# Performance work log

Hardware: AMD Instinct MI355X
Metric: run time of the kernel (lower is better)

The kernel has to match this reference:

```python
import jax, jax.numpy as jnp
import numpy as np

N_NODES = 100000
N_EDGES = 1600000
IN_F, H_F, OUT_F = 32, 32, 16


def setup_inputs() -> dict:
    key = jax.random.key(0)
    ks = jax.random.split(key, 9)
    x = jax.random.normal(ks[0], (N_NODES, IN_F), dtype=jnp.float32)
    src = jax.random.randint(ks[1], (N_EDGES,), 0, N_NODES, dtype=jnp.int32)
    dst = jax.random.randint(ks[2], (N_EDGES,), 0, N_NODES, dtype=jnp.int32)
    W1 = jax.random.normal(ks[3], (IN_F, H_F), dtype=jnp.float32) / np.sqrt(IN_F)
    b1 = jax.random.normal(ks[4], (H_F,), dtype=jnp.float32) * 0.01
    W2 = jax.random.normal(ks[5], (H_F, H_F), dtype=jnp.float32) / np.sqrt(H_F)
    b2 = jax.random.normal(ks[6], (H_F,), dtype=jnp.float32) * 0.01
    W3 = jax.random.normal(ks[7], (H_F, OUT_F), dtype=jnp.float32) / np.sqrt(H_F)
    b3 = jax.random.normal(ks[8], (OUT_F,), dtype=jnp.float32) * 0.01
    return {"x": x, "src": src, "dst": dst,
            "W1": W1, "b1": b1, "W2": W2, "b2": b2, "W3": W3, "b3": b3}


def _gcn_layer(h, src, dst, W, b, num_nodes):
    # copy_u + sum: each dst node accumulates the sum of its source neighbors' features,
    # then dense Linear. Gather-scatter over the edge list (no dense adjacency).
    agg = jax.ops.segment_sum(h[src], dst, num_segments=num_nodes)  # [N, F_in]
    return agg @ W + b


def _leaky_relu(v, slope=0.1):
    return jnp.where(v >= 0, v, slope * v)


def reference(x, src, dst, W1, b1, W2, b2, W3, b3) -> jnp.ndarray:
    n = x.shape[0]
    h = _leaky_relu(_gcn_layer(x, src, dst, W1, b1, n))
    h = _leaky_relu(_gcn_layer(h, src, dst, W2, b2, n))
    return _gcn_layer(h, src, dst, W3, b3, n)  # [N, OUT_F]
```

## Files before the change

kernel.cpp:

```cpp
#include <hip/hip_runtime.h>


#define RANGE_BITS 7
#define RANGE      128
#define MAXBK      1024
#define CHUNK      8192
#define FILL_T     512
#define CSR_T      256
#define CSR_CAP    4096

typedef unsigned short ushort_t;

__device__ __forceinline__ ushort_t f32_to_bf16(float x) {
    unsigned u = __float_as_uint(x);
    u += 0x7fffu + ((u >> 16) & 1u);
    return (ushort_t)(u >> 16);
}
__device__ __forceinline__ float bf16_to_f32(ushort_t h) {
    return __uint_as_float(((unsigned)h) << 16);
}


__global__ void zero_kernel(int* __restrict__ p, int count) {
    int i = blockIdx.x * blockDim.x + threadIdx.x;
    if (i < count) p[i] = 0;
}

__global__ void hist_kernel(const int* __restrict__ dst, int* __restrict__ ghist,
                            int nE, int nbk) {
    __shared__ int h[MAXBK];
    const int tid = threadIdx.x;
    for (int i = tid; i < nbk; i += blockDim.x) h[i] = 0;
    __syncthreads();
    const int stride = gridDim.x * blockDim.x;
    const int nv = nE >> 2;
    const uint4* d4 = (const uint4*)dst;
    for (int i = blockIdx.x * blockDim.x + tid; i < nv; i += stride) {
        uint4 v = d4[i];
        atomicAdd(&h[v.x >> RANGE_BITS], 1);
        atomicAdd(&h[v.y >> RANGE_BITS], 1);
        atomicAdd(&h[v.z >> RANGE_BITS], 1);
        atomicAdd(&h[v.w >> RANGE_BITS], 1);
    }
    for (int e = (nv << 2) + blockIdx.x * blockDim.x + tid; e < nE; e += stride)
        atomicAdd(&h[dst[e] >> RANGE_BITS], 1);
    __syncthreads();
    for (int i = tid; i < nbk; i += blockDim.x) {
        int c = h[i];
        if (c) atomicAdd(&ghist[i], c);
    }
}

__global__ void scan_kernel(int* __restrict__ ghist, int* __restrict__ boff,
                            int* __restrict__ gcur, int nbk) {
    __shared__ int lds[MAXBK];
    const int tid = threadIdx.x;
    for (int i = tid; i < nbk; i += blockDim.x) lds[i] = ghist[i];
    __syncthreads();
    for (int o = 1; o < nbk; o <<= 1) {
        int v = (tid >= o && tid < nbk) ? lds[tid - o] : 0;
        __syncthreads();
        if (tid < nbk) lds[tid] += v;
        __syncthreads();
    }
    if (tid < nbk) {
        int ex = (tid == 0) ? 0 : lds[tid - 1];
        boff[tid] = ex;
        gcur[tid] = ex;
        if (tid == nbk - 1) boff[nbk] = lds[tid];
    }
}

__global__ __launch_bounds__(FILL_T)
void fill_kernel(const int* __restrict__ src, const int* __restrict__ dst,
                 int* __restrict__ gcur, unsigned* __restrict__ edata,
                 int nE, int nbk) {
    __shared__ int cnt[MAXBK];
    __shared__ int base[MAXBK];
    const int tid = threadIdx.x;
    const int c0 = blockIdx.x * CHUNK;
    const int c1 = min(c0 + CHUNK, nE);
    for (int i = tid; i < nbk; i += FILL_T) cnt[i] = 0;
    __syncthreads();
    {
        const int full4 = (c1 - c0) >> 2;
        const uint4* d4 = (const uint4*)(dst + c0);
        for (int i = tid; i < full4; i += FILL_T) {
            uint4 v = d4[i];
            atomicAdd(&cnt[v.x >> RANGE_BITS], 1);
            atomicAdd(&cnt[v.y >> RANGE_BITS], 1);
            atomicAdd(&cnt[v.z >> RANGE_BITS], 1);
            atomicAdd(&cnt[v.w >> RANGE_BITS], 1);
        }
        for (int e = c0 + (full4 << 2) + tid; e < c1; e += FILL_T)
            atomicAdd(&cnt[dst[e] >> RANGE_BITS], 1);
    }
    __syncthreads();
    for (int i = tid; i < nbk; i += FILL_T) {
        int c = cnt[i];
        base[i] = c ? atomicAdd(&gcur[i], c) : 0;
        cnt[i] = 0;
    }
    __syncthreads();
    {
        const int full4 = (c1 - c0) >> 2;
        const uint4* d4 = (const uint4*)(dst + c0);
        const uint4* s4 = (const uint4*)(src + c0);
        for (int i = tid; i < full4; i += FILL_T) {
            uint4 dv = d4[i];
            uint4 sv = s4[i];
#pragma unroll
            for (int u = 0; u < 4; ++u) {
                unsigned d = (&dv.x)[u];
                unsigned s = (&sv.x)[u];
                int bk = (int)(d >> RANGE_BITS);
                int pos = base[bk] + atomicAdd(&cnt[bk], 1);
                edata[pos] = ((d & (RANGE - 1)) << 17) | s;
            }
        }
        for (int e = c0 + (full4 << 2) + tid; e < c1; e += FILL_T) {
            int d = dst[e];
            int bk = d >> RANGE_BITS;
            int pos = base[bk] + atomicAdd(&cnt[bk], 1);
            edata[pos] = ((unsigned)(d & (RANGE - 1)) << 17) | (unsigned)src[e];
        }
    }
}

__global__ __launch_bounds__(CSR_T)
void csr_kernel(const unsigned* __restrict__ edata, const int* __restrict__ boff,
                int* __restrict__ off, int* __restrict__ perm, int n, int nE) {
    __shared__ int hist[RANGE];
    __shared__ int loff[RANGE];
    __shared__ int cur[RANGE];
    __shared__ unsigned stage[CSR_CAP];
    const int tid = threadIdx.x;
    const int rid = blockIdx.x;
    const int e0  = boff[rid];
    const int cnt = boff[rid + 1] - e0;
    const bool fits = cnt <= CSR_CAP;

    if (tid < RANGE) hist[tid] = 0;
    __syncthreads();
    for (int i = tid; i < cnt; i += CSR_T) {
        unsigned p = edata[e0 + i];
        if (fits) stage[i] = p;
        atomicAdd(&hist[p >> 17], 1);
    }
    __syncthreads();
    if (tid < RANGE) loff[tid] = hist[tid];
    __syncthreads();
    for (int o = 1; o < RANGE; o <<= 1) {
        int v = (tid >= o && tid < RANGE) ? loff[tid - o] : 0;
        __syncthreads();
        if (tid < RANGE) loff[tid] += v;
        __syncthreads();
    }
    if (tid < RANGE) {
        int ex = loff[tid] - hist[tid];
        cur[tid] = ex;
        int node = (rid << RANGE_BITS) + tid;
        if (node < n) off[node] = e0 + ex;
    }
    if (tid == 0 && rid == gridDim.x - 1) off[n] = nE;
    __syncthreads();
    for (int i = tid; i < cnt; i += CSR_T) {
        unsigned p = fits ? stage[i] : edata[e0 + i];
        int pos = atomicAdd(&cur[p >> 17], 1);
        perm[e0 + pos] = (int)(p & 0x1ffffu);
    }
}


__global__ void cvt_bf16_kernel(const float* __restrict__ in,
                                ushort_t* __restrict__ out, int total8) {
    int i = blockIdx.x * blockDim.x + threadIdx.x;
    if (i >= total8) return;
    const float4* rp = (const float4*)(in + (size_t)i * 8);
    float4 a = rp[0], b = rp[1];
    uint4 v;
    v.x = (unsigned)f32_to_bf16(a.x) | ((unsigned)f32_to_bf16(a.y) << 16);
    v.y = (unsigned)f32_to_bf16(a.z) | ((unsigned)f32_to_bf16(a.w) << 16);
    v.z = (unsigned)f32_to_bf16(b.x) | ((unsigned)f32_to_bf16(b.y) << 16);
    v.w = (unsigned)f32_to_bf16(b.z) | ((unsigned)f32_to_bf16(b.w) << 16);
    ((uint4*)(out + (size_t)i * 8))[0] = v;
}


template <bool FUSE3>
__global__ __launch_bounds__(256)
void gather_dense_kernel(const ushort_t* __restrict__ t,
                         const int* __restrict__ perm,
                         const int* __restrict__ off,
                         const float* __restrict__ W,
                         const float* __restrict__ b,
                         const float* __restrict__ W3,
                         ushort_t* __restrict__ out,
                         int n) {
    __shared__ float rowbuf[8][33];
    __shared__ float rowbuf2[8][33];
    __shared__ float sW3[32 * 16];
    if (FUSE3) {
        for (int i = threadIdx.x; i < 32 * 16; i += 256) sW3[i] = W3[i];
        __syncthreads();
    }

    const int gid  = blockIdx.x * 256 + threadIdx.x;
    const int node = gid >> 5;
    const int f    = gid & 31;
    const int g    = threadIdx.x >> 5;
    if (node >= n) return;

    const int o = off[node];
    const int d = off[node + 1] - o;
    const int* __restrict__ pp = perm + o;

    float acc = 0.0f;
    for (int base = 0; base < d; base += 32) {
        const int rem = d - base;
        const int m = rem < 32 ? rem : 32;
        int pidx = (f < m) ? pp[base + f] : 0;
        int i = 0;
        for (; i + 15 < m; i += 16) {
            int s[16]; ushort_t v[16];
#pragma unroll
            for (int u = 0; u < 16; ++u) s[u] = __shfl(pidx, i + u, 32);
#pragma unroll
            for (int u = 0; u < 16; ++u) v[u] = t[(s[u] << 5) + f];
#pragma unroll
            for (int u = 0; u < 16; ++u) acc += bf16_to_f32(v[u]);
        }
        for (; i + 7 < m; i += 8) {
            int s[8]; ushort_t v[8];
#pragma unroll
            for (int u = 0; u < 8; ++u) s[u] = __shfl(pidx, i + u, 32);
#pragma unroll
            for (int u = 0; u < 8; ++u) v[u] = t[(s[u] << 5) + f];
#pragma unroll
            for (int u = 0; u < 8; ++u) acc += bf16_to_f32(v[u]);
        }
        for (; i + 3 < m; i += 4) {
            int s[4]; ushort_t v[4];
#pragma unroll
            for (int u = 0; u < 4; ++u) s[u] = __shfl(pidx, i + u, 32);
#pragma unroll
            for (int u = 0; u < 4; ++u) v[u] = t[(s[u] << 5) + f];
#pragma unroll
            for (int u = 0; u < 4; ++u) acc += bf16_to_f32(v[u]);
        }
        for (; i < m; ++i) acc += bf16_to_f32(t[(__shfl(pidx, i, 32) << 5) + f]);
    }

    rowbuf[g][f] = acc;
    float r = b[f];
#pragma unroll
    for (int k = 0; k < 32; ++k) r += rowbuf[g][k] * W[(k << 5) + f];
    r = r >= 0.0f ? r : 0.1f * r;

    if (!FUSE3) {
        out[((size_t)node << 5) + f] = f32_to_bf16(r);
    } else {
        rowbuf2[g][f] = r;
        const int j = f & 15;
        float t3 = 0.0f;
#pragma unroll
        for (int k = 0; k < 32; ++k) t3 += rowbuf2[g][k] * sW3[(k << 4) + j];
        if (f < 16) out[((size_t)node << 4) + f] = f32_to_bf16(t3);
    }
}

__global__ __launch_bounds__(256)
void gather16_kernel(const ushort_t* __restrict__ t3,
                     const int* __restrict__ perm,
                     const int* __restrict__ off,
                     const float* __restrict__ b,
                     float* __restrict__ out,
                     int n) {
    const int gid  = blockIdx.x * 256 + threadIdx.x;
    const int node = gid >> 4;
    const int j    = gid & 15;
    if (node >= n) return;
    const int o = off[node];
    const int d = off[node + 1] - o;
    const int* __restrict__ pp = perm + o;
    float acc = b[j];
    for (int base = 0; base < d; base += 16) {
        const int rem = d - base;
        const int m = rem < 16 ? rem : 16;
        int pidx = (j < m) ? pp[base + j] : 0;
        int i = 0;
        for (; i + 7 < m; i += 8) {
            int s[8]; ushort_t v[8];
#pragma unroll
            for (int u = 0; u < 8; ++u) s[u] = __shfl(pidx, i + u, 16);
#pragma unroll
            for (int u = 0; u < 8; ++u) v[u] = t3[(s[u] << 4) + j];
#pragma unroll
            for (int u = 0; u < 8; ++u) acc += bf16_to_f32(v[u]);
        }
        for (; i < m; ++i) acc += bf16_to_f32(t3[(__shfl(pidx, i, 16) << 4) + j]);
    }
    out[(node << 4) + j] = acc;
}


template <int F>
__global__ void scatter_kernel(const float* __restrict__ h, const int* __restrict__ src,
                               const int* __restrict__ dst, float* __restrict__ agg,
                               int n_edges) {
    int gid = blockIdx.x * blockDim.x + threadIdx.x;
    int e = gid / F, f = gid & (F - 1);
    if (e >= n_edges) return;
    unsafeAtomicAdd(&agg[(size_t)dst[e] * F + f], h[(size_t)src[e] * F + f]);
}

__global__ void zerof_kernel(float* __restrict__ p, int count) {
    int i = blockIdx.x * blockDim.x + threadIdx.x;
    if (i < count) p[i] = 0.0f;
}

template <int IN, int OUT, bool RELU>
__global__ void dense_bias_kernel(const float* __restrict__ in, const float* __restrict__ W,
                                  const float* __restrict__ b, float* __restrict__ out, int n) {
    __shared__ float sW[IN * OUT];
    __shared__ float sb[OUT];
    for (int i = threadIdx.x; i < IN * OUT; i += blockDim.x) sW[i] = W[i];
    for (int i = threadIdx.x; i < OUT; i += blockDim.x) sb[i] = b[i];
    __syncthreads();
    int node = blockIdx.x * blockDim.x + threadIdx.x;
    if (node >= n) return;
    float acc[OUT];
#pragma unroll
    for (int j = 0; j < OUT; ++j) acc[j] = sb[j];
#pragma unroll
    for (int k = 0; k < IN; ++k) {
        float a = in[(size_t)node * IN + k];
#pragma unroll
        for (int j = 0; j < OUT; ++j) acc[j] += a * sW[k * OUT + j];
    }
#pragma unroll
    for (int j = 0; j < OUT; ++j) {
        float v = acc[j];
        out[(size_t)node * OUT + j] = (RELU && v < 0.0f) ? 0.1f * v : v;
    }
}

template <int IN, int OUT>
__global__ void dense_kernel(const float* __restrict__ in, const float* __restrict__ W,
                             float* __restrict__ out, int n) {
    __shared__ float sW[IN * OUT];
    for (int i = threadIdx.x; i < IN * OUT; i += blockDim.x) sW[i] = W[i];
    __syncthreads();
    int node = blockIdx.x * blockDim.x + threadIdx.x;
    if (node >= n) return;
    float acc[OUT];
#pragma unroll
    for (int j = 0; j < OUT; ++j) acc[j] = 0.0f;
#pragma unroll
    for (int k = 0; k < IN; ++k) {
        float a = in[(size_t)node * IN + k];
#pragma unroll
        for (int j = 0; j < OUT; ++j) acc[j] += a * sW[k * OUT + j];
    }
#pragma unroll
    for (int j = 0; j < OUT; ++j) out[(size_t)node * OUT + j] = acc[j];
}

__global__ void init_out_kernel(float* __restrict__ out, const float* __restrict__ b,
                                int total) {
    int gid = blockIdx.x * blockDim.x + threadIdx.x;
    if (gid < total) out[gid] = b[gid & 15];
}


extern "C" void kernel_launch(void* const* d_in, const int* in_sizes, int n_in,
                              void* d_out, int out_size, void* d_ws, size_t ws_size,
                              hipStream_t stream) {
    const float* x  = (const float*)d_in[0];
    const int* src  = (const int*)d_in[1];
    const int* dst  = (const int*)d_in[2];
    const float* W1 = (const float*)d_in[3];
    const float* b1 = (const float*)d_in[4];
    const float* W2 = (const float*)d_in[5];
    const float* b2 = (const float*)d_in[6];
    const float* W3 = (const float*)d_in[7];
    const float* b3 = (const float*)d_in[8];
    float* out = (float*)d_out;

    const int n  = in_sizes[0] / 32;
    const int nE = in_sizes[1];
    const int nbk = (n + RANGE - 1) >> RANGE_BITS;

    unsigned* wsw   = (unsigned*)d_ws;
    ushort_t* xb    = (ushort_t*)wsw;
    ushort_t* h1b   = (ushort_t*)(wsw + (size_t)n * 16);
    ushort_t* t3b   = (ushort_t*)(wsw + (size_t)n * 32);
    unsigned* edata = wsw + (size_t)n * 40;
    int*      perm  = (int*)(edata + nE);
    int*      off   = perm + nE;
    int*      boff  = off + n + 1;
    int*      gcur  = boff + nbk + 1;
    size_t need = ((size_t)n * 40 + 2 * (size_t)nE + (size_t)n + 2 * (size_t)nbk + 2) * 4;

    if (ws_size >= need && nbk <= MAXBK && n < (1 << 17) && (n * 32) % 8 == 0) {
        zero_kernel<<<(nbk + 255) / 256, 256, 0, stream>>>(gcur, nbk);
        hist_kernel<<<256, 512, 0, stream>>>(dst, gcur, nE, nbk);
        cvt_bf16_kernel<<<(n * 32 / 8 + 255) / 256, 256, 0, stream>>>(x, xb, n * 32 / 8);
        scan_kernel<<<1, 1024, 0, stream>>>(gcur, boff, gcur, nbk);
        fill_kernel<<<(nE + CHUNK - 1) / CHUNK, FILL_T, 0, stream>>>(src, dst, gcur, edata, nE, nbk);
        csr_kernel<<<nbk, CSR_T, 0, stream>>>(edata, boff, off, perm, n, nE);

        const int g32 = (n * 32 + 255) / 256;
        const int g16 = (n * 16 + 255) / 256;
        gather_dense_kernel<false><<<g32, 256, 0, stream>>>(xb, perm, off, W1, b1, nullptr, h1b, n);
        gather_dense_kernel<true><<<g32, 256, 0, stream>>>(h1b, perm, off, W2, b2, W3, t3b, n);
        gather16_kernel<<<g16, 256, 0, stream>>>(t3b, perm, off, b3, out, n);
    } else {
        const int BLK = 256;
        const int node_grid = (n + BLK - 1) / BLK;
        float* agg = (float*)d_ws;
        float* h   = agg + (size_t)n * 32;
        zerof_kernel<<<(n * 32 + BLK - 1) / BLK, BLK, 0, stream>>>(agg, n * 32);
        scatter_kernel<32><<<((size_t)nE * 32 + BLK - 1) / BLK, BLK, 0, stream>>>(x, src, dst, agg, nE);
        dense_bias_kernel<32, 32, true><<<node_grid, BLK, 0, stream>>>(agg, W1, b1, h, n);
        zerof_kernel<<<(n * 32 + BLK - 1) / BLK, BLK, 0, stream>>>(agg, n * 32);
        scatter_kernel<32><<<((size_t)nE * 32 + BLK - 1) / BLK, BLK, 0, stream>>>(h, src, dst, agg, nE);
        dense_bias_kernel<32, 32, true><<<node_grid, BLK, 0, stream>>>(agg, W2, b2, h, n);
        dense_kernel<32, 16><<<node_grid, BLK, 0, stream>>>(h, W3, agg, n);
        init_out_kernel<<<(n * 16 + BLK - 1) / BLK, BLK, 0, stream>>>(out, b3, n * 16);
        scatter_kernel<16><<<((size_t)nE * 16 + BLK - 1) / BLK, BLK, 0, stream>>>(agg, src, dst, out, nE);
    }
}
```

Before: 148.6 us.

## Gather bf16 rows with 16-byte vector loads, fewer threads per node

Remaps the gather kernels so each thread loads 8 bf16 features at once as a uint4: 4 threads per node for the 32-wide layers and 2 for the 16-wide layer, instead of one thread per feature. This turns many 2-byte scattered loads into fewer 16-byte loads and moves W into shared memory for the dense step. The trade is less parallelism per node, larger register use per thread, and shared-memory row buffers of 64x33 floats that may reduce occupancy.

```diff
diff --git a/kernel.cpp b/kernel.cpp
--- a/kernel.cpp
+++ b/kernel.cpp
@@ -16,8 +16,11 @@
     u += 0x7fffu + ((u >> 16) & 1u);
     return (ushort_t)(u >> 16);
 }
-__device__ __forceinline__ float bf16_to_f32(ushort_t h) {
-    return __uint_as_float(((unsigned)h) << 16);
+__device__ __forceinline__ float bf16_lo(unsigned w) {
+    return __uint_as_float(w << 16);
+}
+__device__ __forceinline__ float bf16_hi(unsigned w) {
+    return __uint_as_float(w & 0xffff0000u);
 }
 
 
@@ -187,6 +190,13 @@
 }
 
 
+__device__ __forceinline__ void acc_row(float* acc, const uint4& v) {
+    acc[0] += bf16_lo(v.x); acc[1] += bf16_hi(v.x);
+    acc[2] += bf16_lo(v.y); acc[3] += bf16_hi(v.y);
+    acc[4] += bf16_lo(v.z); acc[5] += bf16_hi(v.z);
+    acc[6] += bf16_lo(v.w); acc[7] += bf16_hi(v.w);
+}
+
 template <bool FUSE3>
 __global__ __launch_bounds__(256)
 void gather_dense_kernel(const ushort_t* __restrict__ t,
@@ -197,75 +207,104 @@
                          const float* __restrict__ W3,
                          ushort_t* __restrict__ out,
                          int n) {
-    __shared__ float rowbuf[8][33];
-    __shared__ float rowbuf2[8][33];
+    __shared__ float sW[32 * 32];
     __shared__ float sW3[32 * 16];
-    if (FUSE3) {
-        for (int i = threadIdx.x; i < 32 * 16; i += 256) sW3[i] = W3[i];
-        __syncthreads();
-    }
-
-    const int gid  = blockIdx.x * 256 + threadIdx.x;
-    const int node = gid >> 5;
-    const int f    = gid & 31;
-    const int g    = threadIdx.x >> 5;
+    __shared__ float rowbuf[64][33];
+    __shared__ float rowbuf2[64][33];
+    const int tid = threadIdx.x;
+    for (int i = tid; i < 32 * 32; i += 256) sW[i] = W[i];
+    if (FUSE3)
+        for (int i = tid; i < 32 * 16; i += 256) sW3[i] = W3[i];
+    __syncthreads();
+
+    const int gid  = blockIdx.x * 256 + tid;
+    const int node = gid >> 2;
+    const int f4   = gid & 3;
+    const int lrow = tid >> 2;
     if (node >= n) return;
 
     const int o = off[node];
     const int d = off[node + 1] - o;
     const int* __restrict__ pp = perm + o;
 
-    float acc = 0.0f;
-    for (int base = 0; base < d; base += 32) {
-        const int rem = d - base;
-        const int m = rem < 32 ? rem : 32;
-        int pidx = (f < m) ? pp[base + f] : 0;
-        int i = 0;
-        for (; i + 15 < m; i += 16) {
-            int s[16]; ushort_t v[16];
-#pragma unroll
-            for (int u = 0; u < 16; ++u) s[u] = __shfl(pidx, i + u, 32);
-#pragma unroll
-            for (int u = 0; u < 16; ++u) v[u] = t[(s[u] << 5) + f];
-#pragma unroll
-            for (int u = 0; u < 16; ++u) acc += bf16_to_f32(v[u]);
-        }
-        for (; i + 7 < m; i += 8) {
-            int s[8]; ushort_t v[8];
-#pragma unroll
-            for (int u = 0; u < 8; ++u) s[u] = __shfl(pidx, i + u, 32);
-#pragma unroll
-            for (int u = 0; u < 8; ++u) v[u] = t[(s[u] << 5) + f];
-#pragma unroll
-            for (int u = 0; u < 8; ++u) acc += bf16_to_f32(v[u]);
-        }
-        for (; i + 3 < m; i += 4) {
-            int s[4]; ushort_t v[4];
-#pragma unroll
-            for (int u = 0; u < 4; ++u) s[u] = __shfl(pidx, i + u, 32);
-#pragma unroll
-            for (int u = 0; u < 4; ++u) v[u] = t[(s[u] << 5) + f];
-#pragma unroll
-            for (int u = 0; u < 4; ++u) acc += bf16_to_f32(v[u]);
-        }
-        for (; i < m; ++i) acc += bf16_to_f32(t[(__shfl(pidx, i, 32) << 5) + f]);
-    }
-
-    rowbuf[g][f] = acc;
-    float r = b[f];
-#pragma unroll
-    for (int k = 0; k < 32; ++k) r += rowbuf[g][k] * W[(k << 5) + f];
-    r = r >= 0.0f ? r : 0.1f * r;
+    float acc[8];
+#pragma unroll
+    for (int j = 0; j < 8; ++j) acc[j] = 0.0f;
+
+    int base = 0;
+    for (; base + 8 <= d; base += 8) {
+        int pv0 = pp[base + f4];
+        int pv1 = pp[base + 4 + f4];
+        uint4 v[8];
+#pragma unroll
+        for (int u = 0; u < 4; ++u) {
+            int s = __shfl(pv0, u, 4);
+            v[u] = *((const uint4*)(t + ((size_t)s << 5)) + f4);
+        }
+#pragma unroll
+        for (int u = 0; u < 4; ++u) {
+            int s = __shfl(pv1, u, 4);
+            v[4 + u] = *((const uint4*)(t + ((size_t)s << 5)) + f4);
+        }
+#pragma unroll
+        for (int u = 0; u < 8; ++u) acc_row(acc, v[u]);
+    }
+    if (base + 4 <= d) {
+        int pv = pp[base + f4];
+        uint4 v[4];
+#pragma unroll
+        for (int u = 0; u < 4; ++u) {
+            int s = __shfl(pv, u, 4);
+            v[u] = *((const uint4*)(t + ((size_t)s << 5)) + f4);
+        }
+#pragma unroll
+        for (int u = 0; u < 4; ++u) acc_row(acc, v[u]);
+        base += 4;
+    }
+    for (; base < d; ++base) {
+        int s = pp[base];
+        uint4 v = *((const uint4*)(t + ((size_t)s << 5)) + f4);
+        acc_row(acc, v);
+    }
+
+#pragma unroll
+    for (int j = 0; j < 8; ++j) rowbuf[lrow][f4 * 8 + j] = acc[j];
+
+    float r[8];
+#pragma unroll
+    for (int j = 0; j < 8; ++j) r[j] = b[f4 * 8 + j];
+#pragma unroll
+    for (int k = 0; k < 32; ++k) {
+        float a = rowbuf[lrow][k];
+#pragma unroll
+        for (int j = 0; j < 8; ++j) r[j] += a * sW[(k << 5) + f4 * 8 + j];
+    }
+#pragma unroll
+    for (int j = 0; j < 8; ++j) r[j] = r[j] >= 0.0f ? r[j] : 0.1f * r[j];
 
     if (!FUSE3) {
-        out[((size_t)node << 5) + f] = f32_to_bf16(r);
+        uint4 pk;
+        pk.x = (unsigned)f32_to_bf16(r[0]) | ((unsigned)f32_to_bf16(r[1]) << 16);
+        pk.y = (unsigned)f32_to_bf16(r[2]) | ((unsigned)f32_to_bf16(r[3]) << 16);
+        pk.z = (unsigned)f32_to_bf16(r[4]) | ((unsigned)f32_to_bf16(r[5]) << 16);
+        pk.w = (unsigned)f32_to_bf16(r[6]) | ((unsigned)f32_to_bf16(r[7]) << 16);
+        ((uint4*)(out + ((size_t)node << 5)))[f4] = pk;
     } else {
-        rowbuf2[g][f] = r;
-        const int j = f & 15;
-        float t3 = 0.0f;
-#pragma unroll
-        for (int k = 0; k < 32; ++k) t3 += rowbuf2[g][k] * sW3[(k << 4) + j];
-        if (f < 16) out[((size_t)node << 4) + f] = f32_to_bf16(t3);
+#pragma unroll
+        for (int j = 0; j < 8; ++j) rowbuf2[lrow][f4 * 8 + j] = r[j];
+        float t3v[4];
+#pragma unroll
+        for (int m = 0; m < 4; ++m) t3v[m] = 0.0f;
+#pragma unroll
+        for (int k = 0; k < 32; ++k) {
+            float a = rowbuf2[lrow][k];
+#pragma unroll
+            for (int m = 0; m < 4; ++m) t3v[m] += a * sW3[(k << 4) + f4 * 4 + m];
+        }
+        uint2 pk;
+        pk.x = (unsigned)f32_to_bf16(t3v[0]) | ((unsigned)f32_to_bf16(t3v[1]) << 16);
+        pk.y = (unsigned)f32_to_bf16(t3v[2]) | ((unsigned)f32_to_bf16(t3v[3]) << 16);
+        ((uint2*)(out + ((size_t)node << 4)))[f4] = pk;
     }
 }
 
@@ -277,30 +316,55 @@
                      float* __restrict__ out,
                      int n) {
     const int gid  = blockIdx.x * 256 + threadIdx.x;
-    const int node = gid >> 4;
-    const int j    = gid & 15;
+    const int node = gid >> 1;
+    const int f2   = gid & 1;
     if (node >= n) return;
+
     const int o = off[node];
     const int d = off[node + 1] - o;
     const int* __restrict__ pp = perm + o;
-    float acc = b[j];
-    for (int base = 0; base < d; base += 16) {
-        const int rem = d - base;
-        const int m = rem < 16 ? rem : 16;
-        int pidx = (j < m) ? pp[base + j] : 0;
-        int i = 0;
-        for (; i + 7 < m; i += 8) {
-            int s[8]; ushort_t v[8];
-#pragma unroll
-            for (int u = 0; u < 8; ++u) s[u] = __shfl(pidx, i + u, 16);
-#pragma unroll
-            for (int u = 0; u < 8; ++u) v[u] = t3[(s[u] << 4) + j];
-#pragma unroll
-            for (int u = 0; u < 8; ++u) acc += bf16_to_f32(v[u]);
-        }
-        for (; i < m; ++i) acc += bf16_to_f32(t3[(__shfl(pidx, i, 16) << 4) + j]);
-    }
-    out[(node << 4) + j] = acc;
+
+    float acc[8];
+#pragma unroll
+    for (int j = 0; j < 8; ++j) acc[j] = b[f2 * 8 + j];
+
+    int base = 0;
+    for (; base + 8 <= d; base += 8) {
+        int p0 = pp[base + f2];
+        int p1 = pp[base + 2 + f2];
+        int p2 = pp[base + 4 + f2];
+        int p3 = pp[base + 6 + f2];
+        uint4 v[8];
+        v[0] = *((const uint4*)(t3 + ((size_t)__shfl(p0, 0, 2) << 4)) + f2);
+        v[1] = *((const uint4*)(t3 + ((size_t)__shfl(p0, 1, 2) << 4)) + f2);
+        v[2] = *((const uint4*)(t3 + ((size_t)__shfl(p1, 0, 2) << 4)) + f2);
+        v[3] = *((const uint4*)(t3 + ((size_t)__shfl(p1, 1, 2) << 4)) + f2);
+        v[4] = *((const uint4*)(t3 + ((size_t)__shfl(p2, 0, 2) << 4)) + f2);
+        v[5] = *((const uint4*)(t3 + ((size_t)__shfl(p2, 1, 2) << 4)) + f2);
+        v[6] = *((const uint4*)(t3 + ((size_t)__shfl(p3, 0, 2) << 4)) + f2);
+        v[7] = *((const uint4*)(t3 + ((size_t)__shfl(p3, 1, 2) << 4)) + f2);
+#pragma unroll
+        for (int u = 0; u < 8; ++u) acc_row(acc, v[u]);
+    }
+    for (; base + 2 <= d; base += 2) {
+        int p = pp[base + f2];
+        uint4 v0 = *((const uint4*)(t3 + ((size_t)__shfl(p, 0, 2) << 4)) + f2);
+        uint4 v1 = *((const uint4*)(t3 + ((size_t)__shfl(p, 1, 2) << 4)) + f2);
+        acc_row(acc, v0);
+        acc_row(acc, v1);
+    }
+    if (base < d) {
+        int s = pp[base];
+        uint4 v = *((const uint4*)(t3 + ((size_t)s << 4)) + f2);
+        acc_row(acc, v);
+    }
+
+    float4 o0, o1;
+    o0.x = acc[0]; o0.y = acc[1]; o0.z = acc[2]; o0.w = acc[3];
+    o1.x = acc[4]; o1.y = acc[5]; o1.z = acc[6]; o1.w = acc[7];
+    float4* op = (float4*)(out + ((size_t)node << 4) + f2 * 8);
+    op[0] = o0;
+    op[1] = o1;
 }
 
 
@@ -410,11 +474,11 @@
         fill_kernel<<<(nE + CHUNK - 1) / CHUNK, FILL_T, 0, stream>>>(src, dst, gcur, edata, nE, nbk);
         csr_kernel<<<nbk, CSR_T, 0, stream>>>(edata, boff, off, perm, n, nE);
 
-        const int g32 = (n * 32 + 255) / 256;
-        const int g16 = (n * 16 + 255) / 256;
-        gather_dense_kernel<false><<<g32, 256, 0, stream>>>(xb, perm, off, W1, b1, nullptr, h1b, n);
-        gather_dense_kernel<true><<<g32, 256, 0, stream>>>(h1b, perm, off, W2, b2, W3, t3b, n);
-        gather16_kernel<<<g16, 256, 0, stream>>>(t3b, perm, off, b3, out, n);
+        const int g4 = (n * 4 + 255) / 256;
+        const int g2 = (n * 2 + 255) / 256;
+        gather_dense_kernel<false><<<g4, 256, 0, stream>>>(xb, perm, off, W1, b1, nullptr, h1b, n);
+        gather_dense_kernel<true><<<g4, 256, 0, stream>>>(h1b, perm, off, W2, b2, W3, t3b, n);
+        gather16_kernel<<<g2, 256, 0, stream>>>(t3b, perm, off, b3, out, n);
     } else {
         const int BLK = 256;
         const int node_grid = (n + BLK - 1) / BLK;
```

Result: faster. 125.9 us, median of 2 (-15.3%).
